# Kernel tuning notes

Hardware: AMD Instinct MI355X
Metric: run time of the kernel (lower is better)

The kernel has to match this reference:

```python
import jax, jax.numpy as jnp
import numpy as np

HIDDEN = 1024
HEADS = 16
HEAD = HIDDEN // HEADS
B, S = 2, 2048


def positional_encoding(seq_len, hidden):
    pos = np.arange(seq_len, dtype=np.float32)[:, None]
    div = np.exp(np.arange(0, hidden, 2, dtype=np.float32) * (-np.log(10000.0) / hidden))
    pe = np.zeros((seq_len, hidden), dtype=np.float32)
    pe[:, 0::2] = np.sin(pos * div)
    pe[:, 1::2] = np.cos(pos * div)
    return jnp.asarray(pe)


def setup_inputs() -> dict:
    key = jax.random.key(0)
    ks = jax.random.split(key, 9)
    s = 1.0 / np.sqrt(HIDDEN)
    return {
        "x": jax.random.normal(ks[0], (B, S, HIDDEN), dtype=jnp.float32),
        "Wq": jax.random.normal(ks[1], (HIDDEN, HIDDEN), dtype=jnp.float32) * s,
        "bq": jax.random.normal(ks[2], (HIDDEN,), dtype=jnp.float32) * s,
        "Wk": jax.random.normal(ks[3], (HIDDEN, HIDDEN), dtype=jnp.float32) * s,
        "bk": jax.random.normal(ks[4], (HIDDEN,), dtype=jnp.float32) * s,
        "Wv": jax.random.normal(ks[5], (HIDDEN, HIDDEN), dtype=jnp.float32) * s,
        "bv": jax.random.normal(ks[6], (HIDDEN,), dtype=jnp.float32) * s,
        "Wo": jax.random.normal(ks[7], (HIDDEN, HIDDEN), dtype=jnp.float32) * s,
        "bo": jax.random.normal(ks[8], (HIDDEN,), dtype=jnp.float32) * s,
    }


def reference(x, Wq, bq, Wk, bk, Wv, bv, Wo, bo):
    b, s, _ = x.shape
    x = x + positional_encoding(s, HIDDEN)[None, :, :]
    # torch nn.Linear: y = x @ W.T + b
    q = (x @ Wq.T + bq).reshape(b, s, HEADS, HEAD).transpose(0, 2, 1, 3)  # bhsd
    k = (x @ Wk.T + bk).reshape(b, s, HEADS, HEAD).transpose(0, 2, 1, 3)
    v = (x @ Wv.T + bv).reshape(b, s, HEADS, HEAD).transpose(0, 2, 1, 3)
    scores = jnp.einsum('bhqd,bhkd->bhqk', q, k) / np.sqrt(HEAD).astype(np.float32)
    attn = jax.nn.softmax(scores, axis=-1)
    ctx = jnp.einsum('bhqk,bhkd->bhqd', attn, v)
    ctx = ctx.transpose(0, 2, 1, 3).reshape(b, s, HIDDEN)
    return ctx @ Wo.T + bo
```

## Files before the change

kernel.cpp:

```cpp
#include <hip/hip_runtime.h>
#include <hip/hip_bf16.h>
#include <cstdint>

#define SEQ   2048
#define HID   1024
#define NH    16
#define HD    64
#define NB    2
#define MTOT  (NB*SEQ)

typedef unsigned short u16;
typedef __bf16 bf16x8 __attribute__((ext_vector_type(8)));
typedef float  f32x4  __attribute__((ext_vector_type(4)));
typedef unsigned short u16x8 __attribute__((ext_vector_type(8)));

#if __has_builtin(__builtin_amdgcn_exp2f)
#define EXP2(x) __builtin_amdgcn_exp2f(x)
#else
#define EXP2(x) exp2f(x)
#endif

__device__ __forceinline__ void gll16(const void* g, void* l) {
    __builtin_amdgcn_global_load_lds(
        (const __attribute__((address_space(1))) uint32_t*)(uintptr_t)g,
        (__attribute__((address_space(3))) uint32_t*)(uint32_t)(uintptr_t)l,
        16, 0, 0);
}

__device__ __forceinline__ u16 f2bf(float f) {
    uint32_t u = __builtin_bit_cast(uint32_t, f);
    u += 0x7fffu + ((u >> 16) & 1u);
    return (u16)(u >> 16);
}

__global__ void __launch_bounds__(256) prep_x_kernel(const float* __restrict__ x,
                                                     u16* __restrict__ xpe) {
    int t  = blockIdx.x * 256 + threadIdx.x;
    int i4 = t * 4;
    int m  = i4 >> 10;
    int k0 = i4 & (HID - 1);
    int s  = m & (SEQ - 1);
    const float c = -2.0f * 9.210340371976184f / 1024.0f;
    float4 xv = *(const float4*)(x + i4);
    float vals[4] = {xv.x, xv.y, xv.z, xv.w};
    u16 o[4];
#pragma unroll
    for (int e = 0; e < 4; ++e) {
        int k = k0 + e;
        int i = k >> 1;
        float div = __expf((float)i * c);
        float ang = (float)s * div;
        float pe  = (k & 1) ? __cosf(ang) : __sinf(ang);
        o[e] = f2bf(vals[e] + pe);
    }
    uint2 o2;
    o2.x = (uint32_t)o[0] | ((uint32_t)o[1] << 16);
    o2.y = (uint32_t)o[2] | ((uint32_t)o[3] << 16);
    *(uint2*)(xpe + i4) = o2;
}

__global__ void __launch_bounds__(256) convw4_kernel(const float* __restrict__ s0,
                                                     const float* __restrict__ s1,
                                                     const float* __restrict__ s2,
                                                     const float* __restrict__ s3,
                                                     u16* __restrict__ d0w, u16* __restrict__ d1w,
                                                     u16* __restrict__ d2w, u16* __restrict__ d3w) {
    int z = blockIdx.y;
    const float* src = (z == 0) ? s0 : (z == 1) ? s1 : (z == 2) ? s2 : s3;
    u16* dst = (z == 0) ? d0w : (z == 1) ? d1w : (z == 2) ? d2w : d3w;
    int t  = blockIdx.x * 256 + threadIdx.x;
    int i4 = t * 4;
    float4 v = *(const float4*)(src + i4);
    uint2 o2;
    o2.x = (uint32_t)f2bf(v.x) | ((uint32_t)f2bf(v.y) << 16);
    o2.y = (uint32_t)f2bf(v.z) | ((uint32_t)f2bf(v.w) << 16);
    *(uint2*)(dst + i4) = o2;
}

template <int MODE>
__global__ void __launch_bounds__(256)
gemm128_kernel(const u16* __restrict__ A,
               const u16* __restrict__ B0, const u16* __restrict__ B1, const u16* __restrict__ B2,
               const float* __restrict__ bias0, const float* __restrict__ bias1, const float* __restrict__ bias2,
               void* __restrict__ O0, void* __restrict__ O1, void* __restrict__ O2) {
    const int K = HID;
    __shared__ u16 lds[2][2][128 * 32];
    const int tid  = threadIdx.x;
    const int lane = tid & 63;
    const int wid  = tid >> 6;
    const int n0   = blockIdx.x * 128;
    const int m0   = blockIdx.y * 128;
    const int z    = blockIdx.z;
    const u16*  Bw   = (z == 0) ? B0 : (z == 1) ? B1 : B2;
    const float* bias = (z == 0) ? bias0 : (z == 1) ? bias1 : bias2;

    const int wr = wid >> 1, wc = wid & 1;
    const int l15 = lane & 15, l4 = lane >> 4;

    int offA[4], offB[4];
#pragma unroll
    for (int f = 0; f < 4; ++f) {
        int rA = wr * 64 + f * 16 + l15;
        offA[f] = rA * 64 + ((l4 ^ ((rA >> 1) & 3)) << 4);
        int rB = wc * 64 + f * 16 + l15;
        offB[f] = rB * 64 + ((l4 ^ ((rB >> 1) & 3)) << 4);
    }

    auto stage = [&](int buf, int k0) {
#pragma unroll
        for (int i = 0; i < 2; ++i) {
            int slot = tid + i * 256;
            int row  = slot >> 2;
            int g    = (slot & 3) ^ ((row >> 1) & 3);
            gll16(A  + (size_t)(m0 + row) * K + k0 + g * 8, &lds[buf][0][slot * 8]);
            gll16(Bw + (size_t)(n0 + row) * K + k0 + g * 8, &lds[buf][1][slot * 8]);
        }
    };

    f32x4 acc[4][4] = {};
    stage(0, 0);
    asm volatile("s_waitcnt vmcnt(0)" ::: "memory");
    __syncthreads();
    int cur = 0;
    for (int t = 0; t < K / 32; ++t) {
        if (t + 1 < K / 32) stage(cur ^ 1, (t + 1) * 32);
        const char* baA = (const char*)&lds[cur][0][0];
        const char* baB = (const char*)&lds[cur][1][0];
        bf16x8 af[4], bf[4];
#pragma unroll
        for (int f = 0; f < 4; ++f) af[f] = *(const bf16x8*)(baA + offA[f]);
#pragma unroll
        for (int f = 0; f < 4; ++f) bf[f] = *(const bf16x8*)(baB + offB[f]);
#pragma unroll
        for (int mi = 0; mi < 4; ++mi)
#pragma unroll
            for (int ni = 0; ni < 4; ++ni)
                acc[mi][ni] = __builtin_amdgcn_mfma_f32_16x16x32_bf16(af[mi], bf[ni], acc[mi][ni], 0, 0, 0);
        asm volatile("s_waitcnt vmcnt(0)" ::: "memory");
        __syncthreads();
        cur ^= 1;
    }

    float bi[4];
#pragma unroll
    for (int ni = 0; ni < 4; ++ni) bi[ni] = bias[n0 + wc * 64 + ni * 16 + l15];

    if (MODE == 0) {
        u16* out = (u16*)((z == 0) ? O0 : (z == 1) ? O1 : O2);
        const float scale = (z == 0) ? 0.125f * 1.4426950408889634f : 1.0f;
#pragma unroll
        for (int mi = 0; mi < 4; ++mi)
#pragma unroll
            for (int ni = 0; ni < 4; ++ni) {
                int col = n0 + wc * 64 + ni * 16 + l15;
                int h = col >> 6, d = col & 63;
#pragma unroll
                for (int j = 0; j < 4; ++j) {
                    int row = m0 + wr * 64 + mi * 16 + (l4 << 2) + j;
                    int b = row >> 11, s = row & (SEQ - 1);
                    out[(size_t)((b * NH + h) * SEQ + s) * HD + d] =
                        f2bf((acc[mi][ni][j] + bi[ni]) * scale);
                }
            }
    } else {
        float* out = (float*)O0;
#pragma unroll
        for (int mi = 0; mi < 4; ++mi)
#pragma unroll
            for (int ni = 0; ni < 4; ++ni) {
                int col = n0 + wc * 64 + ni * 16 + l15;
#pragma unroll
                for (int j = 0; j < 4; ++j) {
                    int row = m0 + wr * 64 + mi * 16 + (l4 << 2) + j;
                    out[(size_t)row * HID + col] = acc[mi][ni][j] + bi[ni];
                }
            }
    }
}

__global__ void __launch_bounds__(256, 2)
attn_kernel(const u16* __restrict__ Q, const u16* __restrict__ Kp,
            const u16* __restrict__ V, u16* __restrict__ CTX) {
    __shared__ u16 Klds[2][64 * 64];
    __shared__ u16 Vt[2][64 * 64];
    __shared__ u16 Plds[4][32 * 64];
    const int tid = threadIdx.x, lane = tid & 63, wid = tid >> 6;
    const int l15 = lane & 15, l4 = lane >> 4;
    const int bh = blockIdx.y;
    const size_t base = (size_t)bh * (SEQ * HD);
    const int qw = blockIdx.x * 128 + wid * 32;

    bf16x8 qf[2][2];
#pragma unroll
    for (int g = 0; g < 2; ++g)
#pragma unroll
        for (int kf = 0; kf < 2; ++kf)
            qf[g][kf] = *(const bf16x8*)(Q + base + (size_t)(qw + g * 16 + l15) * HD + kf * 32 + l4 * 8);

    f32x4 acc[2][4] = {};
    float m[2]    = {-__builtin_inff(), -__builtin_inff()};
    float lsum[2] = {0.f, 0.f};

    const int k2 = tid & 31;
    const int d0 = (tid >> 5) * 8;
    u16* Pw = Plds[wid];

    auto stageK = [&](int buf, int kt) {
#pragma unroll
        for (int i = 0; i < 2; ++i) {
            int slot = tid + i * 256;
            int krow = slot >> 3;
            int kg   = (slot & 7) ^ (krow & 7);
            gll16(Kp + base + (size_t)(kt * 64 + krow) * HD + kg * 8,
                  (char*)&Klds[buf][0] + slot * 16);
        }
    };

    auto writeV = [&](int buf, uint4 va, uint4 vb) {
        u16x8 pa = __builtin_bit_cast(u16x8, va);
        u16x8 pb = __builtin_bit_cast(u16x8, vb);
#pragma unroll
        for (int j = 0; j < 8; ++j) {
            uint32_t w = (uint32_t)pa[j] | ((uint32_t)pb[j] << 16);
            *(uint32_t*)((char*)&Vt[buf][0] + (d0 + j) * 128 + ((4 * k2) ^ (j << 4))) = w;
        }
    };

    stageK(0, 0);
    {
        uint4 va = *(const uint4*)(V + base + (size_t)(2 * k2) * HD + d0);
        uint4 vb = *(const uint4*)(V + base + (size_t)(2 * k2 + 1) * HD + d0);
        asm volatile("s_waitcnt vmcnt(0)" ::: "memory");
        writeV(0, va, vb);
    }
    __syncthreads();

    for (int t = 0; t < SEQ / 64; ++t) {
        const int buf = t & 1;
        const bool hn = (t + 1) < SEQ / 64;

        uint4 va, vb;
        if (hn) {
            stageK(buf ^ 1, t + 1);
            va = *(const uint4*)(V + base + (size_t)((t + 1) * 64 + 2 * k2) * HD + d0);
            vb = *(const uint4*)(V + base + (size_t)((t + 1) * 64 + 2 * k2 + 1) * HD + d0);
        }

        f32x4 st[2][4] = {};
        __builtin_amdgcn_s_setprio(1);
#pragma unroll
        for (int ni = 0; ni < 4; ++ni) {
            int kr = ni * 16 + l15;
            const char* kb = (const char*)&Klds[buf][0] + kr * 128;
            bf16x8 k0 = *(const bf16x8*)(kb + ((l4 * 16) ^ ((kr & 7) << 4)));
            bf16x8 k1 = *(const bf16x8*)(kb + ((64 + l4 * 16) ^ ((kr & 7) << 4)));
            st[0][ni] = __builtin_amdgcn_mfma_f32_16x16x32_bf16(k0, qf[0][0], st[0][ni], 0, 0, 0);
            st[0][ni] = __builtin_amdgcn_mfma_f32_16x16x32_bf16(k1, qf[0][1], st[0][ni], 0, 0, 0);
            st[1][ni] = __builtin_amdgcn_mfma_f32_16x16x32_bf16(k0, qf[1][0], st[1][ni], 0, 0, 0);
            st[1][ni] = __builtin_amdgcn_mfma_f32_16x16x32_bf16(k1, qf[1][1], st[1][ni], 0, 0, 0);
        }
        __builtin_amdgcn_s_setprio(0);

#pragma unroll
        for (int g = 0; g < 2; ++g) {
            float pmax = fmaxf(fmaxf(st[g][0][0], st[g][0][1]), fmaxf(st[g][0][2], st[g][0][3]));
#pragma unroll
            for (int ni = 1; ni < 4; ++ni)
                pmax = fmaxf(pmax, fmaxf(fmaxf(st[g][ni][0], st[g][ni][1]),
                                         fmaxf(st[g][ni][2], st[g][ni][3])));
            if (!__all(pmax <= m[g] + 8.0f)) {
                float t0 = fmaxf(pmax, __shfl_xor(pmax, 16));
                t0 = fmaxf(t0, __shfl_xor(t0, 32));
                float mnew  = fmaxf(m[g], t0);
                float alpha = EXP2(m[g] - mnew);
                m[g] = mnew;
                lsum[g] *= alpha;
                float aj[4];
#pragma unroll
                for (int j = 0; j < 4; ++j) aj[j] = __shfl(alpha, l4 * 4 + j, 64);
#pragma unroll
                for (int nd = 0; nd < 4; ++nd)
#pragma unroll
                    for (int j = 0; j < 4; ++j) acc[g][nd][j] *= aj[j];
            }
            float rs = 0.f;
#pragma unroll
            for (int ni = 0; ni < 4; ++ni)
#pragma unroll
                for (int j = 0; j < 4; ++j) {
                    st[g][ni][j] = EXP2(st[g][ni][j] - m[g]);
                    rs += st[g][ni][j];
                }
            lsum[g] += rs;
        }

        if (hn) {
            asm volatile("s_waitcnt vmcnt(0)" ::: "memory");
            writeV(buf ^ 1, va, vb);
        }

#pragma unroll
        for (int g = 0; g < 2; ++g)
#pragma unroll
            for (int ni = 0; ni < 4; ++ni)
#pragma unroll
                for (int jp = 0; jp < 2; ++jp) {
                    uint32_t w;
                    asm("v_cvt_pk_bf16_f32 %0, %1, %2" : "=v"(w)
                        : "v"(st[g][ni][2 * jp]), "v"(st[g][ni][2 * jp + 1]));
                    int key = ni * 16 + l4 * 4 + 2 * jp;
                    *(uint32_t*)((char*)Pw + (g * 16 + l15) * 128 +
                                 ((key * 2) ^ ((l15 & 7) << 4))) = w;
                }

        bf16x8 pf[2][2];
#pragma unroll
        for (int g = 0; g < 2; ++g)
#pragma unroll
            for (int kc = 0; kc < 2; ++kc)
                pf[g][kc] = *(const bf16x8*)((char*)Pw + (g * 16 + l15) * 128 +
                                             ((kc * 64 + l4 * 16) ^ ((l15 & 7) << 4)));

        __builtin_amdgcn_s_setprio(1);
#pragma unroll
        for (int kc = 0; kc < 2; ++kc)
#pragma unroll
            for (int nd = 0; nd < 4; ++nd) {
                int dr = nd * 16 + l15;
                bf16x8 vf = *(const bf16x8*)((char*)&Vt[buf][0] + dr * 128 +
                                             ((kc * 64 + l4 * 16) ^ ((dr & 7) << 4)));
                acc[0][nd] = __builtin_amdgcn_mfma_f32_16x16x32_bf16(pf[0][kc], vf, acc[0][nd], 0, 0, 0);
                acc[1][nd] = __builtin_amdgcn_mfma_f32_16x16x32_bf16(pf[1][kc], vf, acc[1][nd], 0, 0, 0);
            }
        __builtin_amdgcn_s_setprio(0);

        asm volatile("s_waitcnt lgkmcnt(0)" ::: "memory");
        __builtin_amdgcn_s_barrier();
        asm volatile("" ::: "memory");
    }

    const int b = bh >> 4, h = bh & 15;
#pragma unroll
    for (int g = 0; g < 2; ++g) {
        float ls = lsum[g];
        ls += __shfl_xor(ls, 16);
        ls += __shfl_xor(ls, 32);
        float lj[4];
#pragma unroll
        for (int j = 0; j < 4; ++j) lj[j] = 1.0f / __shfl(ls, l4 * 4 + j, 64);
#pragma unroll
        for (int nd = 0; nd < 4; ++nd)
#pragma unroll
            for (int j = 0; j < 4; ++j) {
                int s = qw + g * 16 + l4 * 4 + j;
                int d = nd * 16 + l15;
                CTX[((size_t)(b * SEQ + s)) * HID + h * HD + d] = f2bf(acc[g][nd][j] * lj[j]);
            }
    }
}

extern "C" void kernel_launch(void* const* d_in, const int* in_sizes, int n_in,
                              void* d_out, int out_size, void* d_ws, size_t ws_size,
                              hipStream_t stream) {
    const float* x  = (const float*)d_in[0];
    const float* Wq = (const float*)d_in[1];
    const float* bq = (const float*)d_in[2];
    const float* Wk = (const float*)d_in[3];
    const float* bk = (const float*)d_in[4];
    const float* Wv = (const float*)d_in[5];
    const float* bv = (const float*)d_in[6];
    const float* Wo = (const float*)d_in[7];
    const float* bo = (const float*)d_in[8];
    float* out = (float*)d_out;

    char* ws = (char*)d_ws;
    u16* xpe = (u16*)(ws);
    u16* wqb = (u16*)(ws + ((size_t)8  << 20));
    u16* wkb = (u16*)(ws + ((size_t)10 << 20));
    u16* wvb = (u16*)(ws + ((size_t)12 << 20));
    u16* wob = (u16*)(ws + ((size_t)14 << 20));
    u16* qb  = (u16*)(ws + ((size_t)16 << 20));
    u16* kb  = (u16*)(ws + ((size_t)24 << 20));
    u16* vb  = (u16*)(ws + ((size_t)32 << 20));
    u16* ctx = (u16*)(ws + ((size_t)40 << 20));

    prep_x_kernel<<<dim3(4096), dim3(256), 0, stream>>>(x, xpe);
    convw4_kernel<<<dim3(1024, 4), dim3(256), 0, stream>>>(Wq, Wk, Wv, Wo, wqb, wkb, wvb, wob);

    gemm128_kernel<0><<<dim3(8, 32, 3), dim3(256), 0, stream>>>(
        xpe, wqb, wkb, wvb, bq, bk, bv, qb, kb, vb);

    attn_kernel<<<dim3(16, 32), dim3(256), 0, stream>>>(qb, kb, vb, ctx);

    gemm128_kernel<1><<<dim3(8, 32, 1), dim3(256), 0, stream>>>(
        ctx, wob, wob, wob, bo, bo, bo, out, out, out);
}
```

Measured before the change: 200.9 us.

## Load K fragments directly into registers and swap attention grid axes

```diff
diff --git a/kernel.cpp b/kernel.cpp
--- a/kernel.cpp
+++ b/kernel.cpp
@@ -181,21 +181,20 @@
 __global__ void __launch_bounds__(256, 2)
 attn_kernel(const u16* __restrict__ Q, const u16* __restrict__ Kp,
             const u16* __restrict__ V, u16* __restrict__ CTX) {
-    __shared__ u16 Klds[2][64 * 64];
     __shared__ u16 Vt[2][64 * 64];
     __shared__ u16 Plds[4][32 * 64];
     const int tid = threadIdx.x, lane = tid & 63, wid = tid >> 6;
     const int l15 = lane & 15, l4 = lane >> 4;
-    const int bh = blockIdx.y;
+    const int bh = blockIdx.x;
     const size_t base = (size_t)bh * (SEQ * HD);
-    const int qw = blockIdx.x * 128 + wid * 32;
+    const int q0 = blockIdx.y * 128 + wid * 32;
 
     bf16x8 qf[2][2];
 #pragma unroll
     for (int g = 0; g < 2; ++g)
 #pragma unroll
         for (int kf = 0; kf < 2; ++kf)
-            qf[g][kf] = *(const bf16x8*)(Q + base + (size_t)(qw + g * 16 + l15) * HD + kf * 32 + l4 * 8);
+            qf[g][kf] = *(const bf16x8*)(Q + base + (size_t)(q0 + g * 16 + l15) * HD + kf * 32 + l4 * 8);
 
     f32x4 acc[2][4] = {};
     float m[2]    = {-__builtin_inff(), -__builtin_inff()};
@@ -204,16 +203,16 @@
     const int k2 = tid & 31;
     const int d0 = (tid >> 5) * 8;
     u16* Pw = Plds[wid];
-
-    auto stageK = [&](int buf, int kt) {
-#pragma unroll
-        for (int i = 0; i < 2; ++i) {
-            int slot = tid + i * 256;
-            int krow = slot >> 3;
-            int kg   = (slot & 7) ^ (krow & 7);
-            gll16(Kp + base + (size_t)(kt * 64 + krow) * HD + kg * 8,
-                  (char*)&Klds[buf][0] + slot * 16);
-        }
+    const u16* kPbase = Kp + base + (size_t)l15 * HD + l4 * 8;
+
+    uint4 ka[8];
+    auto loadK = [&](int kt) {
+        const u16* p = kPbase + (size_t)kt * 64 * HD;
+#pragma unroll
+        for (int ni = 0; ni < 4; ++ni)
+#pragma unroll
+            for (int kf = 0; kf < 2; ++kf)
+                ka[ni * 2 + kf] = *(const uint4*)(p + ni * 16 * HD + kf * 32);
     };
 
     auto writeV = [&](int buf, uint4 va, uint4 vb) {
@@ -226,11 +225,10 @@
         }
     };
 
-    stageK(0, 0);
+    loadK(0);
     {
         uint4 va = *(const uint4*)(V + base + (size_t)(2 * k2) * HD + d0);
         uint4 vb = *(const uint4*)(V + base + (size_t)(2 * k2 + 1) * HD + d0);
-        asm volatile("s_waitcnt vmcnt(0)" ::: "memory");
         writeV(0, va, vb);
     }
     __syncthreads();
@@ -241,7 +239,6 @@
 
         uint4 va, vb;
         if (hn) {
-            stageK(buf ^ 1, t + 1);
             va = *(const uint4*)(V + base + (size_t)((t + 1) * 64 + 2 * k2) * HD + d0);
             vb = *(const uint4*)(V + base + (size_t)((t + 1) * 64 + 2 * k2 + 1) * HD + d0);
         }
@@ -250,16 +247,16 @@
         __builtin_amdgcn_s_setprio(1);
 #pragma unroll
         for (int ni = 0; ni < 4; ++ni) {
-            int kr = ni * 16 + l15;
-            const char* kb = (const char*)&Klds[buf][0] + kr * 128;
-            bf16x8 k0 = *(const bf16x8*)(kb + ((l4 * 16) ^ ((kr & 7) << 4)));
-            bf16x8 k1 = *(const bf16x8*)(kb + ((64 + l4 * 16) ^ ((kr & 7) << 4)));
+            bf16x8 k0 = __builtin_bit_cast(bf16x8, ka[ni * 2 + 0]);
+            bf16x8 k1 = __builtin_bit_cast(bf16x8, ka[ni * 2 + 1]);
             st[0][ni] = __builtin_amdgcn_mfma_f32_16x16x32_bf16(k0, qf[0][0], st[0][ni], 0, 0, 0);
             st[0][ni] = __builtin_amdgcn_mfma_f32_16x16x32_bf16(k1, qf[0][1], st[0][ni], 0, 0, 0);
             st[1][ni] = __builtin_amdgcn_mfma_f32_16x16x32_bf16(k0, qf[1][0], st[1][ni], 0, 0, 0);
             st[1][ni] = __builtin_amdgcn_mfma_f32_16x16x32_bf16(k1, qf[1][1], st[1][ni], 0, 0, 0);
         }
         __builtin_amdgcn_s_setprio(0);
+
+        if (hn) loadK(t + 1);
 
 #pragma unroll
         for (int g = 0; g < 2; ++g) {
@@ -294,10 +291,7 @@
             lsum[g] += rs;
         }
 
-        if (hn) {
-            asm volatile("s_waitcnt vmcnt(0)" ::: "memory");
-            writeV(buf ^ 1, va, vb);
-        }
+        if (hn) writeV(buf ^ 1, va, vb);
 
 #pragma unroll
         for (int g = 0; g < 2; ++g)
@@ -352,7 +346,7 @@
         for (int nd = 0; nd < 4; ++nd)
 #pragma unroll
             for (int j = 0; j < 4; ++j) {
-                int s = qw + g * 16 + l4 * 4 + j;
+                int s = q0 + g * 16 + l4 * 4 + j;
                 int d = nd * 16 + l15;
                 CTX[((size_t)(b * SEQ + s)) * HID + h * HD + d] = f2bf(acc[g][nd][j] * lj[j]);
             }
@@ -390,7 +384,7 @@
     gemm128_kernel<0><<<dim3(8, 32, 3), dim3(256), 0, stream>>>(
         xpe, wqb, wkb, wvb, bq, bk, bv, qb, kb, vb);
 
-    attn_kernel<<<dim3(16, 32), dim3(256), 0, stream>>>(qb, kb, vb, ctx);
+    attn_kernel<<<dim3(32, 16), dim3(256), 0, stream>>>(qb, kb, vb, ctx);
 
     gemm128_kernel<1><<<dim3(8, 32, 1), dim3(256), 0, stream>>>(
         ctx, wob, wob, wob, bo, bo, bo, out, out, out);
```

After: 223.6 us. +11.3%, slower.
